# Optimization experiments

Hardware: AMD Instinct MI355X
Metric: run time of the kernel (lower is better)

The kernel has to match this reference:

```python
import jax, jax.numpy as jnp
import numpy as np

N_NODES = 50000
N_EDGES = 1600000
HIDDEN = 128
N_RBF = 50


def _linear_init(key, fan_in, fan_out):
    # mimic torch nn.Linear default init: U(-1/sqrt(fan_in), 1/sqrt(fan_in))
    kw, kb = jax.random.split(key)
    bound = 1.0 / np.sqrt(fan_in)
    W = jax.random.uniform(kw, (fan_in, fan_out), minval=-bound, maxval=bound, dtype=jnp.float32)
    b = jax.random.uniform(kb, (fan_out,), minval=-bound, maxval=bound, dtype=jnp.float32)
    return W, b


def setup_inputs() -> dict:
    key = jax.random.key(0)
    ks = jax.random.split(key, 9)
    x = jax.random.normal(ks[0], (N_NODES, HIDDEN), dtype=jnp.float32)
    edge_index = jax.random.randint(ks[1], (2, N_EDGES), 0, N_NODES, dtype=jnp.int32)
    edge_attr = jax.random.uniform(ks[2], (N_EDGES, N_RBF), dtype=jnp.float32)
    fW1, fb1 = _linear_init(ks[3], N_RBF, HIDDEN)
    fW2, fb2 = _linear_init(ks[4], HIDDEN, HIDDEN)
    dW, db = _linear_init(ks[5], HIDDEN, HIDDEN)
    uW1, ub1 = _linear_init(ks[6], HIDDEN, HIDDEN)
    uW2, ub2 = _linear_init(ks[7], HIDDEN, HIDDEN)
    return {
        "x": x, "edge_index": edge_index, "edge_attr": edge_attr,
        "fW1": fW1, "fb1": fb1, "fW2": fW2, "fb2": fb2,
        "dW": dW, "db": db,
        "uW1": uW1, "ub1": ub1, "uW2": uW2, "ub2": ub2,
    }


def reference(x, edge_index, edge_attr, fW1, fb1, fW2, fb2, dW, db, uW1, ub1, uW2, ub2):
    src, dst = edge_index[0], edge_index[1]
    # filter network: Linear -> SiLU -> Linear on edge RBF features [E, n_rbf] -> [E, H]
    filters = jax.nn.silu(edge_attr @ fW1 + fb1) @ fW2 + fb2
    # messages: dense(x[src]) * filters  [E, H]
    messages = (x[src] @ dW + db) * filters
    # scatter-add to destination nodes
    aggregated = jax.ops.segment_sum(messages, dst, num_segments=x.shape[0])
    # update MLP + residual
    upd = jax.nn.silu(aggregated @ uW1 + ub1) @ uW2 + ub2
    return x + upd
```

## Files before the change

### kernel.cpp

```cpp
#include <hip/hip_runtime.h>

#define H    128
#define RBF  50
#define K1   64
#define EB   64
#define NB   32
#define NBLK 1024

typedef _Float16 f16;
typedef _Float16 f16x4 __attribute__((ext_vector_type(4)));
typedef _Float16 f16x8 __attribute__((ext_vector_type(8)));
typedef float    f32x4 __attribute__((ext_vector_type(4)));

#define HS_LD 136

__device__ __forceinline__ float silu_f(float a) {
    return a / (1.0f + __expf(-a));
}


__global__ __launch_bounds__(256) void prep1_kernel(
    const float* __restrict__ x, const float* __restrict__ dW,
    const float* __restrict__ db, f16* __restrict__ h, int N, int nH,
    const float* __restrict__ fW1, const float* __restrict__ fW2,
    f16* __restrict__ Wt1, f16* __restrict__ Wt2,
    const int* __restrict__ dst, int* __restrict__ counts, int E)
{
    __shared__ float xs[NB][H];
    const int tid = threadIdx.x;
    const int b   = blockIdx.x;

    if (b < nH) {
        const int n0 = b * NB;
        for (int idx = tid; idx < NB * H; idx += 256) {
            int r = idx >> 7, c = idx & (H - 1);
            int n = n0 + r;
            xs[r][c] = (n < N) ? x[(size_t)n * H + c] : 0.f;
        }
        __syncthreads();
        const int j  = tid & (H - 1);
        const int rb = (tid >> 7) * 16;
        float acc[16];
        const float bb = db[j];
#pragma unroll
        for (int r = 0; r < 16; ++r) acc[r] = bb;
        for (int kq = 0; kq < H / 4; ++kq) {
            const int k = kq * 4;
            const float w0 = dW[(k + 0) * H + j];
            const float w1 = dW[(k + 1) * H + j];
            const float w2 = dW[(k + 2) * H + j];
            const float w3 = dW[(k + 3) * H + j];
#pragma unroll
            for (int r = 0; r < 16; ++r) {
                const float4 v = *(const float4*)&xs[rb + r][k];
                acc[r] = fmaf(v.x, w0, fmaf(v.y, w1, fmaf(v.z, w2, fmaf(v.w, w3, acc[r]))));
            }
        }
#pragma unroll
        for (int r = 0; r < 16; ++r) {
            int n = n0 + rb + r;
            if (n < N) h[(size_t)n * H + j] = (f16)acc[r];
        }
    } else if (b < nH + 96) {
        int i = (b - nH) * 256 + tid;
        if (i < H * K1) {
            int n = i >> 6, k = i & (K1 - 1);
            Wt1[i] = (k < RBF) ? (f16)fW1[k * H + n] : (f16)0.f;
        }
        int jj = i - H * K1;
        if (jj >= 0 && jj < H * H) {
            int n = jj >> 7, k = jj & (H - 1);
            Wt2[jj] = (f16)fW2[k * H + n];
        }
    } else {
        const int hb  = b - nH - 96;
        const int hgd = gridDim.x - nH - 96;
        for (int i = hb * 256 + tid; i < E; i += hgd * 256)
            atomicAdd(&counts[dst[i]], 1);
    }
}


__global__ __launch_bounds__(256) void scan1_kernel(
    const int* __restrict__ counts, int* __restrict__ ofs, int* __restrict__ bsum, int N)
{
    __shared__ int s[256];
    const int t = threadIdx.x;
    const int g = blockIdx.x * 256 + t;
    int v = (g < N) ? counts[g] : 0;
    s[t] = v; __syncthreads();
    for (int off = 1; off < 256; off <<= 1) {
        int u = 0; if (t >= off) u = s[t - off];
        __syncthreads(); s[t] += u; __syncthreads();
    }
    if (g < N) ofs[g] = s[t] - v;
    if (t == 255) bsum[blockIdx.x] = s[255];
}
__global__ __launch_bounds__(256) void scan2_kernel(int* __restrict__ bsum, int nb)
{
    __shared__ int s[256];
    const int t = threadIdx.x;
    int v = (t < nb) ? bsum[t] : 0;
    s[t] = v; __syncthreads();
    for (int off = 1; off < 256; off <<= 1) {
        int u = 0; if (t >= off) u = s[t - off];
        __syncthreads(); s[t] += u; __syncthreads();
    }
    if (t < nb) bsum[t] = s[t] - v;
}
__global__ __launch_bounds__(256) void scan3_kernel(
    int* __restrict__ ofs, int* __restrict__ cursor, const int* __restrict__ bsum, int N)
{
    int g = blockIdx.x * 256 + threadIdx.x;
    if (g < N) {
        int v = ofs[g] + bsum[blockIdx.x];
        ofs[g] = v;
        cursor[g] = v;
    }
}

__global__ __launch_bounds__(256) void ranges_kernel(
    const int* __restrict__ ofs, int* __restrict__ nstart, int* __restrict__ estart,
    int N, int E, int B)
{
    int b = blockIdx.x * 256 + threadIdx.x;
    if (b > B) return;
    if (b == B) { nstart[B] = N; estart[B] = E; return; }
    long long cb = (long long)b * E / B;
    int lo = 0, hi = N;
    while (lo < hi) {
        int mid = (lo + hi) >> 1;
        int val = (mid < N) ? ofs[mid] : E;
        if (val < (int)cb) lo = mid + 1; else hi = mid;
    }
    nstart[b] = lo;
    estart[b] = (lo < N) ? ofs[lo] : E;
}

__global__ __launch_bounds__(256) void build_kernel(
    const float* __restrict__ ea, const int* __restrict__ src, const int* __restrict__ dst,
    int* __restrict__ cursor, int2* __restrict__ sd, f16* __restrict__ ea16, int E)
{
    for (int e = blockIdx.x * 256 + threadIdx.x; e < E; e += gridDim.x * 256) {
        const int d = dst[e];
        const int pos = atomicAdd(&cursor[d], 1);
        sd[pos] = make_int2(src[e], d);

        const float* rp = ea + (size_t)e * RBF;
        f16* op = ea16 + (size_t)pos * K1;
        f16x8 v[8];
#pragma unroll
        for (int q = 0; q < 6; ++q) {
            const float4 a = *(const float4*)(rp + q * 8);
            const float4 b = *(const float4*)(rp + q * 8 + 4);
            f16x8 t;
            t[0]=(f16)a.x; t[1]=(f16)a.y; t[2]=(f16)a.z; t[3]=(f16)a.w;
            t[4]=(f16)b.x; t[5]=(f16)b.y; t[6]=(f16)b.z; t[7]=(f16)b.w;
            v[q] = t;
        }
        {
            const float2 a = *(const float2*)(rp + 48);
            f16x8 t = {};
            t[0]=(f16)a.x; t[1]=(f16)a.y;
            v[6] = t;
        }
        v[7] = (f16x8){};
#pragma unroll
        for (int q = 0; q < 8; ++q) *(f16x8*)(op + q * 8) = v[q];
    }
}

__global__ __launch_bounds__(256, 4) void edge_fused_kernel(
    const f16* __restrict__ ea16, const int2* __restrict__ sd,
    const f16* __restrict__ Wt1, const f16* __restrict__ Wt2,
    const float* __restrict__ fb1, const float* __restrict__ fb2,
    const f16* __restrict__ h, float* __restrict__ out,
    const int* __restrict__ nstart, const int* __restrict__ estart)
{
    __shared__ __align__(16) f16 uni[8192];
    __shared__ __align__(16) f16 h_s[EB * HS_LD];
    __shared__ int src_s[2][EB];
    __shared__ int dst_s[2][EB];

    const int tid  = threadIdx.x;
    const int lane = tid & 63;
    const int wv   = tid >> 6;
    const int wr   = (wv >> 1) * 32;
    const int wc   = (wv & 1) * 64;
    const int fr   = lane & 15;
    const int qw   = lane >> 4;
    const int kb   = qw * 8;

    const int j = tid >> 2;
    const int s = tid & 3;

    f16x8 B1[4][2];
    f16x8 B2[4][4];
    float b1v[4], b2v[4];
#pragma unroll
    for (int ct = 0; ct < 4; ++ct) {
        const int col = wc + ct * 16 + fr;
#pragma unroll
        for (int ks = 0; ks < 2; ++ks)
            B1[ct][ks] = *(const f16x8*)&Wt1[col * K1 + ks * 32 + kb];
#pragma unroll
        for (int ks = 0; ks < 4; ++ks)
            B2[ct][ks] = *(const f16x8*)&Wt2[col * H + ks * 32 + kb];
        b1v[ct] = fb1[col];
        b2v[ct] = fb2[col];
    }

    const int ns = nstart[blockIdx.x], ne = nstart[blockIdx.x + 1];
    const int e0 = estart[blockIdx.x], e1 = estart[blockIdx.x + 1];

    if (e0 >= e1) {
        for (int idx = tid; idx < (ne - ns) * H; idx += 256)
            out[(size_t)ns * H + idx] = 0.f;
        return;
    }

    const int col128 = tid & 127;
    int   curdst = ns;
    float accv   = 0.f;
    int   cur    = 0;

    if (tid < EB) {
        int idx = e0 + tid; idx = (idx < e1) ? idx : (e1 - 1);
        int2 v = sd[idx];
        src_s[0][tid] = v.x;
        dst_s[0][tid] = (e0 + tid < e1) ? v.y : ne;
    }
    __syncthreads();

    for (int tb = e0; tb < e1; tb += EB) {
        {
#pragma unroll
            for (int i = 0; i < 2; ++i) {
                const int row = (tid >> 3) + i * 32;
                const int ch  = tid & 7;
                const f16* hp = h + (size_t)src_s[cur][row] * H;
#pragma unroll
                for (int half = 0; half < 2; ++half)
                    *(f16x8*)&h_s[row * HS_LD + half * 64 + ch * 8] =
                        *(const f16x8*)(hp + half * 64 + ch * 8);
            }
            const int pe = tb + j;
            const f16* ep = ea16 + (size_t)((pe < e1) ? pe : (e1 - 1)) * K1;
            const f16x8 ev1 = *(const f16x8*)(ep + s * 8);
            const f16x8 ev2 = *(const f16x8*)(ep + 32 + s * 8);
            *(f16x8*)((char*)uni + (size_t)(((s)     * 64 + j) * 16)) = ev1;
            *(f16x8*)((char*)uni + (size_t)(((4 + s) * 64 + j) * 16)) = ev2;
        }
        __syncthreads();

        f32x4 acc1[2][4];
#pragma unroll
        for (int rt = 0; rt < 2; ++rt)
#pragma unroll
            for (int ct = 0; ct < 4; ++ct)
                acc1[rt][ct] = (f32x4){b1v[ct], b1v[ct], b1v[ct], b1v[ct]};
#pragma unroll
        for (int ks = 0; ks < 2; ++ks) {
            const f16x8 A0 = *(const f16x8*)((char*)uni + (size_t)(((ks * 4 + qw) * 64 + wr + fr) * 16));
            const f16x8 A1 = *(const f16x8*)((char*)uni + (size_t)(((ks * 4 + qw) * 64 + wr + 16 + fr) * 16));
#pragma unroll
            for (int ct = 0; ct < 4; ++ct) {
                acc1[0][ct] = __builtin_amdgcn_mfma_f32_16x16x32_f16(A0, B1[ct][ks], acc1[0][ct], 0, 0, 0);
                acc1[1][ct] = __builtin_amdgcn_mfma_f32_16x16x32_f16(A1, B1[ct][ks], acc1[1][ct], 0, 0, 0);
            }
        }
        __syncthreads();

#pragma unroll
        for (int rt = 0; rt < 2; ++rt)
#pragma unroll
            for (int ct = 0; ct < 4; ++ct)
#pragma unroll
                for (int m = 0; m < 4; ++m) {
                    const int er = wr + rt * 16 + qw * 4 + m;
                    const int c  = wc + ct * 16 + fr;
                    *(f16*)((char*)uni + (size_t)(((c >> 3) * 64 + er) * 16 + (c & 7) * 2)) =
                        (f16)silu_f(acc1[rt][ct][m]);
                }
        __syncthreads();

        f32x4 acc2[2][4];
#pragma unroll
        for (int rt = 0; rt < 2; ++rt)
#pragma unroll
            for (int ct = 0; ct < 4; ++ct)
                acc2[rt][ct] = (f32x4){b2v[ct], b2v[ct], b2v[ct], b2v[ct]};
#pragma unroll
        for (int ks = 0; ks < 4; ++ks) {
            const f16x8 A0 = *(const f16x8*)((char*)uni + (size_t)(((ks * 4 + qw) * 64 + wr + fr) * 16));
            const f16x8 A1 = *(const f16x8*)((char*)uni + (size_t)(((ks * 4 + qw) * 64 + wr + 16 + fr) * 16));
#pragma unroll
            for (int ct = 0; ct < 4; ++ct) {
                acc2[0][ct] = __builtin_amdgcn_mfma_f32_16x16x32_f16(A0, B2[ct][ks], acc2[0][ct], 0, 0, 0);
                acc2[1][ct] = __builtin_amdgcn_mfma_f32_16x16x32_f16(A1, B2[ct][ks], acc2[1][ct], 0, 0, 0);
            }
        }

#pragma unroll
        for (int rt = 0; rt < 2; ++rt)
#pragma unroll
            for (int ct = 0; ct < 4; ++ct)
#pragma unroll
                for (int m = 0; m < 4; ++m) {
                    const int er = wr + rt * 16 + qw * 4 + m;
                    const int c  = wc + ct * 16 + fr;
                    f16* p = &h_s[er * HS_LD + c];
                    *p = (f16)((float)*p * acc2[rt][ct][m]);
                }
        __syncthreads();

        if (tid < 128) {
            const int* ds = dst_s[cur];
            for (int r = 0; r < EB; ++r) {
                const int d = ds[r];
                const float v = (float)h_s[r * HS_LD + col128];
                if (d != curdst) {
                    out[(size_t)curdst * H + col128] = accv;
                    for (int n = curdst + 1; n < d; ++n) out[(size_t)n * H + col128] = 0.f;
                    curdst = d; accv = 0.f;
                }
                if (d < ne) accv += v;
            }
        } else if (tid < 128 + EB) {
            const int r = tid - 128;
            int idx = tb + EB + r; idx = (idx < e1) ? idx : (e1 - 1);
            int2 v = sd[idx];
            src_s[cur ^ 1][r] = v.x;
            dst_s[cur ^ 1][r] = (tb + EB + r < e1) ? v.y : ne;
        }
        __syncthreads();

        cur ^= 1;
    }

    if (tid < 128 && curdst < ne) {
        out[(size_t)curdst * H + col128] = accv;
        for (int n = curdst + 1; n < ne; ++n) out[(size_t)n * H + col128] = 0.f;
    }
}

__global__ __launch_bounds__(256) void update_kernel(
    const float* __restrict__ x,
    const float* __restrict__ uW1, const float* __restrict__ ub1,
    const float* __restrict__ uW2, const float* __restrict__ ub2,
    float* __restrict__ out, int N)
{
    __shared__ float as[NB][H];
    __shared__ float ts[NB][H];
    const int tid = threadIdx.x;
    const int n0  = blockIdx.x * NB;
    for (int idx = tid; idx < NB * H; idx += 256) {
        int r = idx >> 7, c = idx & (H - 1);
        int n = n0 + r;
        as[r][c] = (n < N) ? out[(size_t)n * H + c] : 0.f;
    }
    __syncthreads();
    const int j  = tid & (H - 1);
    const int rb = (tid >> 7) * 16;
    float acc[16];
    {
        const float b1 = ub1[j];
#pragma unroll
        for (int r = 0; r < 16; ++r) acc[r] = b1;
    }
    for (int kq = 0; kq < H / 4; ++kq) {
        const int k = kq * 4;
        const float w0 = uW1[(k + 0) * H + j];
        const float w1 = uW1[(k + 1) * H + j];
        const float w2 = uW1[(k + 2) * H + j];
        const float w3 = uW1[(k + 3) * H + j];
#pragma unroll
        for (int r = 0; r < 16; ++r) {
            const float4 v = *(const float4*)&as[rb + r][k];
            acc[r] = fmaf(v.x, w0, fmaf(v.y, w1, fmaf(v.z, w2, fmaf(v.w, w3, acc[r]))));
        }
    }
#pragma unroll
    for (int r = 0; r < 16; ++r) ts[rb + r][j] = silu_f(acc[r]);
    __syncthreads();
    {
        const float b2 = ub2[j];
#pragma unroll
        for (int r = 0; r < 16; ++r) acc[r] = b2;
    }
    for (int kq = 0; kq < H / 4; ++kq) {
        const int k = kq * 4;
        const float w0 = uW2[(k + 0) * H + j];
        const float w1 = uW2[(k + 1) * H + j];
        const float w2 = uW2[(k + 2) * H + j];
        const float w3 = uW2[(k + 3) * H + j];
#pragma unroll
        for (int r = 0; r < 16; ++r) {
            const float4 v = *(const float4*)&ts[rb + r][k];
            acc[r] = fmaf(v.x, w0, fmaf(v.y, w1, fmaf(v.z, w2, fmaf(v.w, w3, acc[r]))));
        }
    }
#pragma unroll
    for (int r = 0; r < 16; ++r) {
        int n = n0 + rb + r;
        if (n < N) out[(size_t)n * H + j] = x[(size_t)n * H + j] + acc[r];
    }
}

extern "C" void kernel_launch(void* const* d_in, const int* in_sizes, int n_in,
                              void* d_out, int out_size, void* d_ws, size_t ws_size,
                              hipStream_t stream) {
    const float* x   = (const float*)d_in[0];
    const int*   ei  = (const int*)  d_in[1];
    const float* ea  = (const float*)d_in[2];
    const float* fW1 = (const float*)d_in[3];
    const float* fb1 = (const float*)d_in[4];
    const float* fW2 = (const float*)d_in[5];
    const float* fb2 = (const float*)d_in[6];
    const float* dW  = (const float*)d_in[7];
    const float* db  = (const float*)d_in[8];
    const float* uW1 = (const float*)d_in[9];
    const float* ub1 = (const float*)d_in[10];
    const float* uW2 = (const float*)d_in[11];
    const float* ub2 = (const float*)d_in[12];

    float* out = (float*)d_out;
    const int N = in_sizes[0] / H;
    const int E = in_sizes[1] / 2;
    const int* src = ei;
    const int* dst = ei + E;

    char* ws = (char*)d_ws;
    size_t off = 0;
    auto alloc = [&](size_t bytes) { void* p = ws + off; off = (off + bytes + 255) & ~(size_t)255; return p; };
    f16*  h      = (f16*) alloc((size_t)N * H * sizeof(f16));
    f16*  Wt1    = (f16*) alloc((size_t)H * K1 * sizeof(f16));
    f16*  Wt2    = (f16*) alloc((size_t)H * H * sizeof(f16));
    int*  counts = (int*) alloc((size_t)N * sizeof(int));
    int*  ofs    = (int*) alloc((size_t)N * sizeof(int));
    int*  cursor = (int*) alloc((size_t)N * sizeof(int));
    int*  bsum   = (int*) alloc(256 * sizeof(int));
    int*  nstart = (int*) alloc((size_t)(NBLK + 1) * sizeof(int));
    int*  estart = (int*) alloc((size_t)(NBLK + 1) * sizeof(int));
    int2* sd     = (int2*)alloc((size_t)E * sizeof(int2));
    f16*  ea16   = (f16*) alloc((size_t)E * K1 * sizeof(f16));

    const int nH    = (N + NB - 1) / NB;
    const int nscan = (N + 255) / 256;

    hipMemsetAsync(counts, 0, (size_t)N * sizeof(int), stream);

    prep1_kernel<<<nH + 96 + 2048, 256, 0, stream>>>(
        x, dW, db, h, N, nH, fW1, fW2, Wt1, Wt2, dst, counts, E);

    scan1_kernel<<<nscan, 256, 0, stream>>>(counts, ofs, bsum, N);
    scan2_kernel<<<1, 256, 0, stream>>>(bsum, nscan);
    scan3_kernel<<<nscan, 256, 0, stream>>>(ofs, cursor, bsum, N);

    ranges_kernel<<<(NBLK + 256) / 256, 256, 0, stream>>>(ofs, nstart, estart, N, E, NBLK);

    build_kernel<<<2048, 256, 0, stream>>>(ea, src, dst, cursor, sd, ea16, E);

    edge_fused_kernel<<<NBLK, 256, 0, stream>>>(
        ea16, sd, Wt1, Wt2, fb1, fb2, h, out, nstart, estart);

    update_kernel<<<nH, 256, 0, stream>>>(
        x, uW1, ub1, uW2, ub2, out, N);
}
```

Baseline: 894.1 us.

## Sort edges by source for message GEMM, then reduce materialized messages by destination

Edges are now bucketed by source node as well as destination, so the message kernel reads h rows with locality. Each message is written to a dst-sorted fp16 buffer, and a separate reduce kernel does the segmented sum per destination. If workspace is too small, the code falls back to float atomics into a zeroed output. This adds a second counting sort, a scatter of E×H fp16 messages, an extra pass to reread them, and more atomics in the build kernel.

```diff
diff --git a/kernel.cpp b/kernel.cpp
--- a/kernel.cpp
+++ b/kernel.cpp
@@ -8,7 +8,6 @@
 #define NBLK 1024
 
 typedef _Float16 f16;
-typedef _Float16 f16x4 __attribute__((ext_vector_type(4)));
 typedef _Float16 f16x8 __attribute__((ext_vector_type(8)));
 typedef float    f32x4 __attribute__((ext_vector_type(4)));
 
@@ -17,14 +16,14 @@
 __device__ __forceinline__ float silu_f(float a) {
     return a / (1.0f + __expf(-a));
 }
-
 
 __global__ __launch_bounds__(256) void prep1_kernel(
     const float* __restrict__ x, const float* __restrict__ dW,
     const float* __restrict__ db, f16* __restrict__ h, int N, int nH,
     const float* __restrict__ fW1, const float* __restrict__ fW2,
     f16* __restrict__ Wt1, f16* __restrict__ Wt2,
-    const int* __restrict__ dst, int* __restrict__ counts, int E)
+    const int* __restrict__ src, const int* __restrict__ dst,
+    int* __restrict__ counts2, int E)
 {
     __shared__ float xs[NB][H];
     const int tid = threadIdx.x;
@@ -75,79 +74,99 @@
     } else {
         const int hb  = b - nH - 96;
         const int hgd = gridDim.x - nH - 96;
-        for (int i = hb * 256 + tid; i < E; i += hgd * 256)
-            atomicAdd(&counts[dst[i]], 1);
+        for (int i = hb * 256 + tid; i < E; i += hgd * 256) {
+            atomicAdd(&counts2[src[i]], 1);
+            atomicAdd(&counts2[N + dst[i]], 1);
+        }
     }
 }
 
 
 __global__ __launch_bounds__(256) void scan1_kernel(
-    const int* __restrict__ counts, int* __restrict__ ofs, int* __restrict__ bsum, int N)
+    const int* __restrict__ counts, int* __restrict__ ofs, int* __restrict__ bsum, int N2)
 {
     __shared__ int s[256];
     const int t = threadIdx.x;
     const int g = blockIdx.x * 256 + t;
-    int v = (g < N) ? counts[g] : 0;
+    int v = (g < N2) ? counts[g] : 0;
     s[t] = v; __syncthreads();
     for (int off = 1; off < 256; off <<= 1) {
         int u = 0; if (t >= off) u = s[t - off];
         __syncthreads(); s[t] += u; __syncthreads();
     }
-    if (g < N) ofs[g] = s[t] - v;
+    if (g < N2) ofs[g] = s[t] - v;
     if (t == 255) bsum[blockIdx.x] = s[255];
 }
-__global__ __launch_bounds__(256) void scan2_kernel(int* __restrict__ bsum, int nb)
+__global__ __launch_bounds__(256) void scan2c_kernel(int* __restrict__ bsum, int nb)
 {
     __shared__ int s[256];
     const int t = threadIdx.x;
-    int v = (t < nb) ? bsum[t] : 0;
-    s[t] = v; __syncthreads();
+    const int C = (nb + 255) / 256;
+    const int b0 = min(t * C, nb), b1 = min(b0 + C, nb);
+    int sum = 0;
+    for (int i = b0; i < b1; ++i) sum += bsum[i];
+    s[t] = sum; __syncthreads();
     for (int off = 1; off < 256; off <<= 1) {
         int u = 0; if (t >= off) u = s[t - off];
         __syncthreads(); s[t] += u; __syncthreads();
     }
-    if (t < nb) bsum[t] = s[t] - v;
+    int run = (t > 0) ? s[t - 1] : 0;
+    for (int i = b0; i < b1; ++i) { int v = bsum[i]; bsum[i] = run; run += v; }
 }
 __global__ __launch_bounds__(256) void scan3_kernel(
-    int* __restrict__ ofs, int* __restrict__ cursor, const int* __restrict__ bsum, int N)
+    int* __restrict__ ofs, int* __restrict__ cursor, const int* __restrict__ bsum, int N2)
 {
     int g = blockIdx.x * 256 + threadIdx.x;
-    if (g < N) {
+    if (g < N2) {
         int v = ofs[g] + bsum[blockIdx.x];
         ofs[g] = v;
         cursor[g] = v;
     }
 }
 
-__global__ __launch_bounds__(256) void ranges_kernel(
+__global__ __launch_bounds__(256) void post_scan_kernel(
     const int* __restrict__ ofs, int* __restrict__ nstart, int* __restrict__ estart,
-    int N, int E, int B)
-{
-    int b = blockIdx.x * 256 + threadIdx.x;
-    if (b > B) return;
-    if (b == B) { nstart[B] = N; estart[B] = E; return; }
-    long long cb = (long long)b * E / B;
-    int lo = 0, hi = N;
-    while (lo < hi) {
-        int mid = (lo + hi) >> 1;
-        int val = (mid < N) ? ofs[mid] : E;
-        if (val < (int)cb) lo = mid + 1; else hi = mid;
-    }
-    nstart[b] = lo;
-    estart[b] = (lo < N) ? ofs[lo] : E;
-}
-
+    int* __restrict__ dstarr, int N, int E, int B, int RB, int doFill)
+{
+    if ((int)blockIdx.x < RB) {
+        int b = blockIdx.x * 256 + threadIdx.x;
+        if (b > B) return;
+        if (b == B) { nstart[B] = N; estart[B] = E; return; }
+        long long cb = (long long)b * E / B;
+        int lo = 0, hi = N;
+        while (lo < hi) {
+            int mid = (lo + hi) >> 1;
+            int val = (mid < N) ? (ofs[N + mid] - E) : E;
+            if (val < (int)cb) lo = mid + 1; else hi = mid;
+        }
+        nstart[b] = lo;
+        estart[b] = (lo < N) ? (ofs[N + lo] - E) : E;
+    } else if (doFill) {
+        const int stride = (gridDim.x - RB) * 256;
+        for (int n = (blockIdx.x - RB) * 256 + threadIdx.x; n < N; n += stride) {
+            const int a   = ofs[N + n] - E;
+            const int bnd = (n == N - 1) ? E : (ofs[N + n + 1] - E);
+            for (int j = a; j < bnd; ++j) dstarr[j] = n;
+        }
+    }
+}
+
+template<int MAT>
 __global__ __launch_bounds__(256) void build_kernel(
     const float* __restrict__ ea, const int* __restrict__ src, const int* __restrict__ dst,
-    int* __restrict__ cursor, int2* __restrict__ sd, f16* __restrict__ ea16, int E)
+    int* __restrict__ cursor, int2* __restrict__ aux, f16* __restrict__ eaS, int N, int E)
 {
     for (int e = blockIdx.x * 256 + threadIdx.x; e < E; e += gridDim.x * 256) {
-        const int d = dst[e];
-        const int pos = atomicAdd(&cursor[d], 1);
-        sd[pos] = make_int2(src[e], d);
+        const int sN = src[e];
+        const int d  = dst[e];
+        const int posS = atomicAdd(&cursor[sN], 1);
+        int aux_y;
+        if (MAT) aux_y = atomicAdd(&cursor[N + d], 1) - E;
+        else     aux_y = d;
+        aux[posS] = make_int2(sN, aux_y);
 
         const float* rp = ea + (size_t)e * RBF;
-        f16* op = ea16 + (size_t)pos * K1;
+        f16* op = eaS + (size_t)posS * K1;
         f16x8 v[8];
 #pragma unroll
         for (int q = 0; q < 6; ++q) {
@@ -170,17 +189,18 @@
     }
 }
 
-__global__ __launch_bounds__(256, 4) void edge_fused_kernel(
-    const f16* __restrict__ ea16, const int2* __restrict__ sd,
+template<int MAT>
+__global__ __launch_bounds__(256, 4) void msg_kernel(
+    const f16* __restrict__ eaS, const int2* __restrict__ aux,
     const f16* __restrict__ Wt1, const f16* __restrict__ Wt2,
     const float* __restrict__ fb1, const float* __restrict__ fb2,
-    const f16* __restrict__ h, float* __restrict__ out,
-    const int* __restrict__ nstart, const int* __restrict__ estart)
+    const f16* __restrict__ h, f16* __restrict__ msg, float* __restrict__ out,
+    int E, int ntiles)
 {
     __shared__ __align__(16) f16 uni[8192];
     __shared__ __align__(16) f16 h_s[EB * HS_LD];
-    __shared__ int src_s[2][EB];
-    __shared__ int dst_s[2][EB];
+    __shared__ int src_s[EB];
+    __shared__ int aux_s[EB];
 
     const int tid  = threadIdx.x;
     const int lane = tid & 63;
@@ -210,42 +230,31 @@
         b2v[ct] = fb2[col];
     }
 
-    const int ns = nstart[blockIdx.x], ne = nstart[blockIdx.x + 1];
-    const int e0 = estart[blockIdx.x], e1 = estart[blockIdx.x + 1];
-
-    if (e0 >= e1) {
-        for (int idx = tid; idx < (ne - ns) * H; idx += 256)
-            out[(size_t)ns * H + idx] = 0.f;
-        return;
-    }
-
-    const int col128 = tid & 127;
-    int   curdst = ns;
-    float accv   = 0.f;
-    int   cur    = 0;
-
-    if (tid < EB) {
-        int idx = e0 + tid; idx = (idx < e1) ? idx : (e1 - 1);
-        int2 v = sd[idx];
-        src_s[0][tid] = v.x;
-        dst_s[0][tid] = (e0 + tid < e1) ? v.y : ne;
-    }
-    __syncthreads();
-
-    for (int tb = e0; tb < e1; tb += EB) {
+    for (int t = blockIdx.x; t < ntiles; t += gridDim.x) {
+        const int tb = t * EB;
+        __syncthreads();
+
+        if (tid < EB) {
+            int idx = tb + tid;
+            int2 a = aux[(idx < E) ? idx : (E - 1)];
+            src_s[tid] = a.x;
+            aux_s[tid] = (idx < E) ? a.y : -1;
+        }
+        __syncthreads();
+
         {
 #pragma unroll
             for (int i = 0; i < 2; ++i) {
                 const int row = (tid >> 3) + i * 32;
                 const int ch  = tid & 7;
-                const f16* hp = h + (size_t)src_s[cur][row] * H;
+                const f16* hp = h + (size_t)src_s[row] * H;
 #pragma unroll
                 for (int half = 0; half < 2; ++half)
                     *(f16x8*)&h_s[row * HS_LD + half * 64 + ch * 8] =
                         *(const f16x8*)(hp + half * 64 + ch * 8);
             }
             const int pe = tb + j;
-            const f16* ep = ea16 + (size_t)((pe < e1) ? pe : (e1 - 1)) * K1;
+            const f16* ep = eaS + (size_t)((pe < E) ? pe : (E - 1)) * K1;
             const f16x8 ev1 = *(const f16x8*)(ep + s * 8);
             const f16x8 ev2 = *(const f16x8*)(ep + 32 + s * 8);
             *(f16x8*)((char*)uni + (size_t)(((s)     * 64 + j) * 16)) = ev1;
@@ -314,8 +323,76 @@
                 }
         __syncthreads();
 
+        if (MAT) {
+#pragma unroll
+            for (int i = 0; i < 2; ++i) {
+                const int row = (tid >> 3) + i * 32;
+                const int ch  = tid & 7;
+                const int pd  = aux_s[row];
+                if (pd >= 0) {
+#pragma unroll
+                    for (int half = 0; half < 2; ++half)
+                        *(f16x8*)&msg[(size_t)pd * H + half * 64 + ch * 8] =
+                            *(const f16x8*)&h_s[row * HS_LD + half * 64 + ch * 8];
+                }
+            }
+        } else {
+#pragma unroll
+            for (int i = 0; i < 2; ++i) {
+                const int row = (tid >> 3) + i * 32;
+                const int ch  = tid & 7;
+                const int d   = aux_s[row];
+                if (d >= 0) {
+#pragma unroll
+                    for (int half = 0; half < 2; ++half)
+#pragma unroll
+                        for (int k2 = 0; k2 < 8; ++k2) {
+                            const int c = half * 64 + ch * 8 + k2;
+                            unsafeAtomicAdd(&out[(size_t)d * H + c],
+                                            (float)h_s[row * HS_LD + c]);
+                        }
+                }
+            }
+        }
+    }
+}
+
+__global__ __launch_bounds__(256, 4) void reduce_kernel(
+    const f16* __restrict__ msg, const int* __restrict__ dstarr,
+    float* __restrict__ out,
+    const int* __restrict__ nstart, const int* __restrict__ estart)
+{
+    __shared__ __align__(16) f16 h_s[EB * HS_LD];
+    __shared__ int ds[EB];
+
+    const int tid = threadIdx.x;
+    const int ns = nstart[blockIdx.x], ne = nstart[blockIdx.x + 1];
+    const int e0 = estart[blockIdx.x], e1 = estart[blockIdx.x + 1];
+
+    if (e0 >= e1) {
+        for (int idx = tid; idx < (ne - ns) * H; idx += 256)
+            out[(size_t)ns * H + idx] = 0.f;
+        return;
+    }
+
+    const int col128 = tid & 127;
+    int   curdst = ns;
+    float accv   = 0.f;
+
+    for (int tb = e0; tb < e1; tb += EB) {
+#pragma unroll
+        for (int it = 0; it < 4; ++it) {
+            const int idx = tid + it * 256;
+            const int row = idx >> 4;
+            const int c8  = (idx & 15) * 8;
+            const int gr  = tb + row;
+            if (gr < e1)
+                *(f16x8*)&h_s[row * HS_LD + c8] = *(const f16x8*)&msg[(size_t)gr * H + c8];
+        }
+        if (tid < EB) ds[tid] = (tb + tid < e1) ? dstarr[tb + tid] : ne;
+        __syncthreads();
+
         if (tid < 128) {
-            const int* ds = dst_s[cur];
             for (int r = 0; r < EB; ++r) {
                 const int d = ds[r];
                 const float v = (float)h_s[r * HS_LD + col128];
@@ -326,16 +403,8 @@
                 }
                 if (d < ne) accv += v;
             }
-        } else if (tid < 128 + EB) {
-            const int r = tid - 128;
-            int idx = tb + EB + r; idx = (idx < e1) ? idx : (e1 - 1);
-            int2 v = sd[idx];
-            src_s[cur ^ 1][r] = v.x;
-            dst_s[cur ^ 1][r] = (tb + EB + r < e1) ? v.y : ne;
-        }
-        __syncthreads();
-
-        cur ^= 1;
+        }
+        __syncthreads();
     }
 
     if (tid < 128 && curdst < ne) {
@@ -429,40 +498,55 @@
     const int E = in_sizes[1] / 2;
     const int* src = ei;
     const int* dst = ei + E;
+    const int N2 = 2 * N;
 
     char* ws = (char*)d_ws;
     size_t off = 0;
     auto alloc = [&](size_t bytes) { void* p = ws + off; off = (off + bytes + 255) & ~(size_t)255; return p; };
-    f16*  h      = (f16*) alloc((size_t)N * H * sizeof(f16));
-    f16*  Wt1    = (f16*) alloc((size_t)H * K1 * sizeof(f16));
-    f16*  Wt2    = (f16*) alloc((size_t)H * H * sizeof(f16));
-    int*  counts = (int*) alloc((size_t)N * sizeof(int));
-    int*  ofs    = (int*) alloc((size_t)N * sizeof(int));
-    int*  cursor = (int*) alloc((size_t)N * sizeof(int));
-    int*  bsum   = (int*) alloc(256 * sizeof(int));
-    int*  nstart = (int*) alloc((size_t)(NBLK + 1) * sizeof(int));
-    int*  estart = (int*) alloc((size_t)(NBLK + 1) * sizeof(int));
-    int2* sd     = (int2*)alloc((size_t)E * sizeof(int2));
-    f16*  ea16   = (f16*) alloc((size_t)E * K1 * sizeof(f16));
-
-    const int nH    = (N + NB - 1) / NB;
-    const int nscan = (N + 255) / 256;
-
-    hipMemsetAsync(counts, 0, (size_t)N * sizeof(int), stream);
+    f16*  h       = (f16*) alloc((size_t)N * H * sizeof(f16));
+    f16*  Wt1     = (f16*) alloc((size_t)H * K1 * sizeof(f16));
+    f16*  Wt2     = (f16*) alloc((size_t)H * H * sizeof(f16));
+    int*  counts2 = (int*) alloc((size_t)N2 * sizeof(int));
+    int*  ofs     = (int*) alloc((size_t)N2 * sizeof(int));
+    int*  cursor  = (int*) alloc((size_t)N2 * sizeof(int));
+    int*  bsum    = (int*) alloc(2048 * sizeof(int));
+    int*  nstart  = (int*) alloc((size_t)(NBLK + 1) * sizeof(int));
+    int*  estart  = (int*) alloc((size_t)(NBLK + 1) * sizeof(int));
+    int2* aux     = (int2*)alloc((size_t)E * sizeof(int2));
+    int*  dstarr  = (int*) alloc((size_t)E * sizeof(int));
+    f16*  eaS     = (f16*) alloc((size_t)E * K1 * sizeof(f16));
+    size_t base = off;
+    f16*  msg     = (f16*)(ws + base);
+    const bool MAT = (ws_size >= base + (size_t)E * H * sizeof(f16));
+
+    const int nH     = (N + NB - 1) / NB;
+    const int nscan  = (N2 + 255) / 256;
+    const int ntiles = (E + EB - 1) / EB;
+    const int RB     = (NBLK + 1 + 255) / 256;
+
+    hipMemsetAsync(counts2, 0, (size_t)N2 * sizeof(int), stream);
+    if (!MAT) hipMemsetAsync(out, 0, (size_t)N * H * sizeof(float), stream);
 
     prep1_kernel<<<nH + 96 + 2048, 256, 0, stream>>>(
-        x, dW, db, h, N, nH, fW1, fW2, Wt1, Wt2, dst, counts, E);
-
-    scan1_kernel<<<nscan, 256, 0, stream>>>(counts, ofs, bsum, N);
-    scan2_kernel<<<1, 256, 0, stream>>>(bsum, nscan);
-    scan3_kernel<<<nscan, 256, 0, stream>>>(ofs, cursor, bsum, N);
-
-    ranges_kernel<<<(NBLK + 256) / 256, 256, 0, stream>>>(ofs, nstart, estart, N, E, NBLK);
-
-    build_kernel<<<2048, 256, 0, stream>>>(ea, src, dst, cursor, sd, ea16, E);
-
-    edge_fused_kernel<<<NBLK, 256, 0, stream>>>(
-        ea16, sd, Wt1, Wt2, fb1, fb2, h, out, nstart, estart);
+        x, dW, db, h, N, nH, fW1, fW2, Wt1, Wt2, src, dst, counts2, E);
+
+    scan1_kernel<<<nscan, 256, 0, stream>>>(counts2, ofs, bsum, N2);
+    scan2c_kernel<<<1, 256, 0, stream>>>(bsum, nscan);
+    scan3_kernel<<<nscan, 256, 0, stream>>>(ofs, cursor, bsum, N2);
+
+    post_scan_kernel<<<RB + 200, 256, 0, stream>>>(
+        ofs, nstart, estart, dstarr, N, E, NBLK, RB, MAT ? 1 : 0);
+
+    if (MAT) {
+        build_kernel<1><<<2048, 256, 0, stream>>>(ea, src, dst, cursor, aux, eaS, N, E);
+        msg_kernel<1><<<NBLK, 256, 0, stream>>>(
+            eaS, aux, Wt1, Wt2, fb1, fb2, h, msg, out, E, ntiles);
+        reduce_kernel<<<NBLK, 256, 0, stream>>>(msg, dstarr, out, nstart, estart);
+    } else {
+        build_kernel<0><<<2048, 256, 0, stream>>>(ea, src, dst, cursor, aux, eaS, N, E);
+        msg_kernel<0><<<NBLK, 256, 0, stream>>>(
+            eaS, aux, Wt1, Wt2, fb1, fb2, h, (f16*)nullptr, out, E, ntiles);
+    }
 
     update_kernel<<<nH, 256, 0, stream>>>(
         x, uW1, ub1, uW2, ub2, out, N);
```

New measurement: 1.133 ms. 26.7% more time.

## Group edges within each block by source range to improve gather locality

Applied to the files above, without the earlier changes.

Edges inside each block's range are now ordered first by source-node group (four groups split by source index), then by destination. This is meant to shrink the working set of the h[src] gathers in the fused edge kernel and improve cache hit rate. Because a destination's edges now appear as up to four separate runs, the output is zero-initialized first and partial sums are accumulated with read-modify-write. Extra counting atomics, a second scan over a 4N array, and two additional setup kernels add launch and memory-traffic overhead.

```diff
diff --git a/kernel.cpp b/kernel.cpp
--- a/kernel.cpp
+++ b/kernel.cpp
@@ -6,9 +6,9 @@
 #define EB   64
 #define NB   32
 #define NBLK 1024
+#define GS   4
 
 typedef _Float16 f16;
-typedef _Float16 f16x4 __attribute__((ext_vector_type(4)));
 typedef _Float16 f16x8 __attribute__((ext_vector_type(8)));
 typedef float    f32x4 __attribute__((ext_vector_type(4)));
 
@@ -16,6 +16,9 @@
 
 __device__ __forceinline__ float silu_f(float a) {
     return a / (1.0f + __expf(-a));
+}
+__device__ __forceinline__ int groupof(int s, int N) {
+    return (int)(((long long)s * GS) / N);
 }
 
 
@@ -24,7 +27,8 @@
     const float* __restrict__ db, f16* __restrict__ h, int N, int nH,
     const float* __restrict__ fW1, const float* __restrict__ fW2,
     f16* __restrict__ Wt1, f16* __restrict__ Wt2,
-    const int* __restrict__ dst, int* __restrict__ counts, int E)
+    const int* __restrict__ src, const int* __restrict__ dst,
+    int* __restrict__ cnt_d, int* __restrict__ cnt_gd, int E)
 {
     __shared__ float xs[NB][H];
     const int tid = threadIdx.x;
@@ -75,49 +79,54 @@
     } else {
         const int hb  = b - nH - 96;
         const int hgd = gridDim.x - nH - 96;
-        for (int i = hb * 256 + tid; i < E; i += hgd * 256)
-            atomicAdd(&counts[dst[i]], 1);
+        for (int i = hb * 256 + tid; i < E; i += hgd * 256) {
+            const int dV = dst[i];
+            const int g  = groupof(src[i], N);
+            atomicAdd(&cnt_d[dV], 1);
+            atomicAdd(&cnt_gd[g * N + dV], 1);
+        }
     }
 }
 
 
 __global__ __launch_bounds__(256) void scan1_kernel(
-    const int* __restrict__ counts, int* __restrict__ ofs, int* __restrict__ bsum, int N)
+    const int* __restrict__ counts, int* __restrict__ ofs, int* __restrict__ bsum, int M)
 {
     __shared__ int s[256];
     const int t = threadIdx.x;
     const int g = blockIdx.x * 256 + t;
-    int v = (g < N) ? counts[g] : 0;
+    int v = (g < M) ? counts[g] : 0;
     s[t] = v; __syncthreads();
     for (int off = 1; off < 256; off <<= 1) {
         int u = 0; if (t >= off) u = s[t - off];
         __syncthreads(); s[t] += u; __syncthreads();
     }
-    if (g < N) ofs[g] = s[t] - v;
+    if (g < M) ofs[g] = s[t] - v;
     if (t == 255) bsum[blockIdx.x] = s[255];
 }
-__global__ __launch_bounds__(256) void scan2_kernel(int* __restrict__ bsum, int nb)
+__global__ __launch_bounds__(256) void scan2c_kernel(int* __restrict__ bsum, int nb)
 {
     __shared__ int s[256];
     const int t = threadIdx.x;
-    int v = (t < nb) ? bsum[t] : 0;
-    s[t] = v; __syncthreads();
+    const int C = (nb + 255) / 256;
+    const int b0 = min(t * C, nb), b1 = min(b0 + C, nb);
+    int sum = 0;
+    for (int i = b0; i < b1; ++i) sum += bsum[i];
+    s[t] = sum; __syncthreads();
     for (int off = 1; off < 256; off <<= 1) {
         int u = 0; if (t >= off) u = s[t - off];
         __syncthreads(); s[t] += u; __syncthreads();
     }
-    if (t < nb) bsum[t] = s[t] - v;
+    int run = (t > 0) ? s[t - 1] : 0;
+    for (int i = b0; i < b1; ++i) { int v = bsum[i]; bsum[i] = run; run += v; }
 }
 __global__ __launch_bounds__(256) void scan3_kernel(
-    int* __restrict__ ofs, int* __restrict__ cursor, const int* __restrict__ bsum, int N)
+    int* __restrict__ ofs, const int* __restrict__ bsum, int M)
 {
     int g = blockIdx.x * 256 + threadIdx.x;
-    if (g < N) {
-        int v = ofs[g] + bsum[blockIdx.x];
-        ofs[g] = v;
-        cursor[g] = v;
-    }
-}
+    if (g < M) ofs[g] += bsum[blockIdx.x];
+}
+
 
 __global__ __launch_bounds__(256) void ranges_kernel(
     const int* __restrict__ ofs, int* __restrict__ nstart, int* __restrict__ estart,
@@ -137,14 +146,50 @@
     estart[b] = (lo < N) ? ofs[lo] : E;
 }
 
+__global__ __launch_bounds__(256) void nbfill_kernel(
+    const int* __restrict__ nstart, int* __restrict__ nb, int N)
+{
+    int n = blockIdx.x * 256 + threadIdx.x;
+    if (n >= N) return;
+    int lo = 0, hi = NBLK - 1;
+    while (lo < hi) {
+        int mid = (lo + hi + 1) >> 1;
+        if (nstart[mid] <= n) lo = mid; else hi = mid - 1;
+    }
+    nb[n] = lo;
+}
+
+__global__ __launch_bounds__(256) void cursor_init_kernel(
+    const int* __restrict__ P, const int* __restrict__ nb,
+    const int* __restrict__ nstart, const int* __restrict__ estart,
+    int* __restrict__ cursor_gd, int N)
+{
+    int idx = blockIdx.x * 256 + threadIdx.x;
+    if (idx >= GS * N) return;
+    const int g = idx / N;
+    const int d = idx - g * N;
+    const int b  = nb[d];
+    const int ns = nstart[b];
+    const int ne = nstart[b + 1];
+    int base = estart[b];
+#pragma unroll
+    for (int gp = 0; gp < GS - 1; ++gp)
+        if (gp < g)
+            base += P[gp * N + ne] - P[gp * N + ns];
+    base += P[g * N + d] - P[g * N + ns];
+    cursor_gd[idx] = base;
+}
+
 __global__ __launch_bounds__(256) void build_kernel(
     const float* __restrict__ ea, const int* __restrict__ src, const int* __restrict__ dst,
-    int* __restrict__ cursor, int2* __restrict__ sd, f16* __restrict__ ea16, int E)
+    int* __restrict__ cursor_gd, int2* __restrict__ sd, f16* __restrict__ ea16, int N, int E)
 {
     for (int e = blockIdx.x * 256 + threadIdx.x; e < E; e += gridDim.x * 256) {
-        const int d = dst[e];
-        const int pos = atomicAdd(&cursor[d], 1);
-        sd[pos] = make_int2(src[e], d);
+        const int sV = src[e];
+        const int d  = dst[e];
+        const int g  = groupof(sV, N);
+        const int pos = atomicAdd(&cursor_gd[g * N + d], 1);
+        sd[pos] = make_int2(sV, d);
 
         const float* rp = ea + (size_t)e * RBF;
         f16* op = ea16 + (size_t)pos * K1;
@@ -213,11 +258,9 @@
     const int ns = nstart[blockIdx.x], ne = nstart[blockIdx.x + 1];
     const int e0 = estart[blockIdx.x], e1 = estart[blockIdx.x + 1];
 
-    if (e0 >= e1) {
-        for (int idx = tid; idx < (ne - ns) * H; idx += 256)
-            out[(size_t)ns * H + idx] = 0.f;
-        return;
-    }
+    for (int idx = tid; idx < (ne - ns) * H; idx += 256)
+        out[(size_t)ns * H + idx] = 0.f;
+    if (e0 >= e1) return;
 
     const int col128 = tid & 127;
     int   curdst = ns;
@@ -320,8 +363,7 @@
                 const int d = ds[r];
                 const float v = (float)h_s[r * HS_LD + col128];
                 if (d != curdst) {
-                    out[(size_t)curdst * H + col128] = accv;
-                    for (int n = curdst + 1; n < d; ++n) out[(size_t)n * H + col128] = 0.f;
+                    if (curdst < ne) out[(size_t)curdst * H + col128] += accv;
                     curdst = d; accv = 0.f;
                 }
                 if (d < ne) accv += v;
@@ -338,10 +380,8 @@
         cur ^= 1;
     }
 
-    if (tid < 128 && curdst < ne) {
-        out[(size_t)curdst * H + col128] = accv;
-        for (int n = curdst + 1; n < ne; ++n) out[(size_t)n * H + col128] = 0.f;
-    }
+    if (tid < 128 && curdst < ne)
+        out[(size_t)curdst * H + col128] += accv;
 }
 
 __global__ __launch_bounds__(256) void update_kernel(
@@ -429,37 +469,51 @@
     const int E = in_sizes[1] / 2;
     const int* src = ei;
     const int* dst = ei + E;
+    const int SN = GS * N;
 
     char* ws = (char*)d_ws;
     size_t off = 0;
     auto alloc = [&](size_t bytes) { void* p = ws + off; off = (off + bytes + 255) & ~(size_t)255; return p; };
-    f16*  h      = (f16*) alloc((size_t)N * H * sizeof(f16));
-    f16*  Wt1    = (f16*) alloc((size_t)H * K1 * sizeof(f16));
-    f16*  Wt2    = (f16*) alloc((size_t)H * H * sizeof(f16));
-    int*  counts = (int*) alloc((size_t)N * sizeof(int));
-    int*  ofs    = (int*) alloc((size_t)N * sizeof(int));
-    int*  cursor = (int*) alloc((size_t)N * sizeof(int));
-    int*  bsum   = (int*) alloc(256 * sizeof(int));
-    int*  nstart = (int*) alloc((size_t)(NBLK + 1) * sizeof(int));
-    int*  estart = (int*) alloc((size_t)(NBLK + 1) * sizeof(int));
-    int2* sd     = (int2*)alloc((size_t)E * sizeof(int2));
-    f16*  ea16   = (f16*) alloc((size_t)E * K1 * sizeof(f16));
-
-    const int nH    = (N + NB - 1) / NB;
-    const int nscan = (N + 255) / 256;
-
-    hipMemsetAsync(counts, 0, (size_t)N * sizeof(int), stream);
+    f16*  h         = (f16*) alloc((size_t)N * H * sizeof(f16));
+    f16*  Wt1       = (f16*) alloc((size_t)H * K1 * sizeof(f16));
+    f16*  Wt2       = (f16*) alloc((size_t)H * H * sizeof(f16));
+    int*  cnt_d     = (int*) alloc((size_t)N * sizeof(int));
+    int*  ofs       = (int*) alloc((size_t)N * sizeof(int));
+    int*  cnt_gd    = (int*) alloc((size_t)SN * sizeof(int));
+    int*  P         = (int*) alloc((size_t)SN * sizeof(int));
+    int*  cursor_gd = (int*) alloc((size_t)SN * sizeof(int));
+    int*  nb        = (int*) alloc((size_t)N * sizeof(int));
+    int*  bsum      = (int*) alloc(1024 * sizeof(int));
+    int*  bsum2     = (int*) alloc(2048 * sizeof(int));
+    int*  nstart    = (int*) alloc((size_t)(NBLK + 1) * sizeof(int));
+    int*  estart    = (int*) alloc((size_t)(NBLK + 1) * sizeof(int));
+    int2* sd        = (int2*)alloc((size_t)E * sizeof(int2));
+    f16*  ea16      = (f16*) alloc((size_t)E * K1 * sizeof(f16));
+
+    const int nH       = (N + NB - 1) / NB;
+    const int nscan_d  = (N + 255) / 256;
+    const int nscan_gd = (SN + 255) / 256;
+
+    hipMemsetAsync(cnt_d,  0, (size_t)N  * sizeof(int), stream);
+    hipMemsetAsync(cnt_gd, 0, (size_t)SN * sizeof(int), stream);
 
     prep1_kernel<<<nH + 96 + 2048, 256, 0, stream>>>(
-        x, dW, db, h, N, nH, fW1, fW2, Wt1, Wt2, dst, counts, E);
-
-    scan1_kernel<<<nscan, 256, 0, stream>>>(counts, ofs, bsum, N);
-    scan2_kernel<<<1, 256, 0, stream>>>(bsum, nscan);
-    scan3_kernel<<<nscan, 256, 0, stream>>>(ofs, cursor, bsum, N);
+        x, dW, db, h, N, nH, fW1, fW2, Wt1, Wt2, src, dst, cnt_d, cnt_gd, E);
+
+    scan1_kernel<<<nscan_d, 256, 0, stream>>>(cnt_d, ofs, bsum, N);
+    scan2c_kernel<<<1, 256, 0, stream>>>(bsum, nscan_d);
+    scan3_kernel<<<nscan_d, 256, 0, stream>>>(ofs, bsum, N);
+
+    scan1_kernel<<<nscan_gd, 256, 0, stream>>>(cnt_gd, P, bsum2, SN);
+    scan2c_kernel<<<1, 256, 0, stream>>>(bsum2, nscan_gd);
+    scan3_kernel<<<nscan_gd, 256, 0, stream>>>(P, bsum2, SN);
 
     ranges_kernel<<<(NBLK + 256) / 256, 256, 0, stream>>>(ofs, nstart, estart, N, E, NBLK);
-
-    build_kernel<<<2048, 256, 0, stream>>>(ea, src, dst, cursor, sd, ea16, E);
+    nbfill_kernel<<<(N + 255) / 256, 256, 0, stream>>>(nstart, nb, N);
+    cursor_init_kernel<<<(SN + 255) / 256, 256, 0, stream>>>(
+        P, nb, nstart, estart, cursor_gd, N);
+
+    build_kernel<<<2048, 256, 0, stream>>>(ea, src, dst, cursor_gd, sd, ea16, N, E);
 
     edge_fused_kernel<<<NBLK, 256, 0, stream>>>(
         ea16, sd, Wt1, Wt2, fb1, fb2, h, out, nstart, estart);
```

After: 1.027 ms. +14.9%, slower.
